# Kernel optimization log

Measured on AMD Instinct MI355X. Metric: run time of the kernel, lower is better.

The kernel has to match this reference:

```python
import jax, jax.numpy as jnp
import numpy as np

N_STATE = 1024
N_HEAD = 16
B = 2
S = 2048


def setup_inputs() -> dict:
    key = jax.random.key(0)
    ks = jax.random.split(key, 8)
    s = 0.02
    x = jax.random.normal(ks[0], (B, S, N_STATE), dtype=jnp.float32)
    # causal additive mask, as in Whisper: upper triangle = -inf
    mask = jnp.where(jnp.triu(jnp.ones((S, S), dtype=bool), k=1), -jnp.inf, 0.0).astype(jnp.float32)
    Wq = jax.random.normal(ks[1], (N_STATE, N_STATE), dtype=jnp.float32) * s
    bq = jax.random.normal(ks[2], (N_STATE,), dtype=jnp.float32) * s
    Wk = jax.random.normal(ks[3], (N_STATE, N_STATE), dtype=jnp.float32) * s
    Wv = jax.random.normal(ks[4], (N_STATE, N_STATE), dtype=jnp.float32) * s
    bv = jax.random.normal(ks[5], (N_STATE,), dtype=jnp.float32) * s
    Wo = jax.random.normal(ks[6], (N_STATE, N_STATE), dtype=jnp.float32) * s
    bo = jax.random.normal(ks[7], (N_STATE,), dtype=jnp.float32) * s
    return {"x": x, "mask": mask, "Wq": Wq, "bq": bq, "Wk": Wk,
            "Wv": Wv, "bv": bv, "Wo": Wo, "bo": bo}


def reference(x, mask, Wq, bq, Wk, Wv, bv, Wo, bo):
    Bb, S_, D = x.shape
    H = N_HEAD
    hd = D // H
    scale = hd ** (-0.25)  # scale split across q and k, as in the source
    q = x @ Wq.T + bq              # [B,S,D]
    k = x @ Wk.T                   # key has no bias
    v = x @ Wv.T + bv
    # [B,S,D] -> [B,H,S,hd]
    q = q.reshape(Bb, S_, H, hd).transpose(0, 2, 1, 3) * scale
    k = k.reshape(Bb, S_, H, hd).transpose(0, 2, 1, 3) * scale
    v = v.reshape(Bb, S_, H, hd).transpose(0, 2, 1, 3)
    qk = jnp.einsum('bhsd,bhtd->bhst', q, k) + mask[:S_, :S_]
    w = jax.nn.softmax(qk, axis=-1).astype(q.dtype)
    out = jnp.einsum('bhst,bhtd->bhsd', w, v)
    out = out.transpose(0, 2, 1, 3).reshape(Bb, S_, D)
    return out @ Wo.T + bo
```

## Files before the change

kernel.cpp:

```cpp
#include <hip/hip_runtime.h>
#include <hip/hip_bf16.h>
#include <cmath>

typedef __bf16 bf16;
typedef __bf16 bf16x8 __attribute__((ext_vector_type(8)));
typedef __bf16 bf16x4 __attribute__((ext_vector_type(4)));
typedef float f32x4 __attribute__((ext_vector_type(4)));

#define QS 0.18033688f

__device__ __forceinline__ void load16_to_lds(const void* g, void* l) {
    __builtin_amdgcn_global_load_lds(
        (const __attribute__((address_space(1))) unsigned int*)g,
        (__attribute__((address_space(3))) unsigned int*)l, 16, 0, 0);
}

__global__ __launch_bounds__(256) void convert_kernel(
    const float* __restrict__ x,  const float* __restrict__ wq,
    const float* __restrict__ wk, const float* __restrict__ wv,
    const float* __restrict__ wo, bf16* __restrict__ dst)
{
    const size_t M1 = 1024ull * 1024ull, M4 = 4ull * M1;
    size_t i0 = ((size_t)blockIdx.x * 256 + threadIdx.x) * 8;
    const float* s;
    size_t off;
    float sc = 1.f;
    if      (i0 < M4)        { s = x;  off = i0; }
    else if (i0 < M4 + M1)   { s = wq; off = i0 - M4; sc = QS; }
    else if (i0 < M4 + 2*M1) { s = wk; off = i0 - M4 - M1; }
    else if (i0 < M4 + 3*M1) { s = wv; off = i0 - M4 - 2*M1; }
    else                     { s = wo; off = i0 - M4 - 3*M1; }
    float4 a = *(const float4*)(s + off);
    float4 b = *(const float4*)(s + off + 4);
    bf16x8 r = { (bf16)(a.x*sc), (bf16)(a.y*sc), (bf16)(a.z*sc), (bf16)(a.w*sc),
                 (bf16)(b.x*sc), (bf16)(b.y*sc), (bf16)(b.z*sc), (bf16)(b.w*sc) };
    *(bf16x8*)(dst + i0) = r;
}

template<int BM, bool OUT_F32>
__device__ __forceinline__ void gemm_core(
    const bf16* __restrict__ A, const bf16* __restrict__ W,
    const float* __restrict__ bias, void* __restrict__ C,
    int mb, int nb, bool vt_out, float bias_scale)
{
    constexpr int IF = BM / 32;
    __shared__ __align__(16) bf16 As[BM * 32];
    __shared__ __align__(16) bf16 Bs[128 * 32];

    const int tid  = threadIdx.x;
    const int lane = tid & 63;
    const int wave = tid >> 6;
    const int wr   = (wave >> 1) * (BM / 2);
    const int wc   = (wave & 1) * 64;
    const int l15  = lane & 15;
    const int l4   = lane >> 4;
    const int swz  = (l4 ^ ((l15 >> 1) & 3)) * 8;

    f32x4 acc[IF][4] = {};

    for (int kt = 0; kt < 32; ++kt) {
#pragma unroll
        for (int it = 0; it < BM / 64; ++it) {
            int c = it * 256 + tid;
            int scol = ((c & 3) ^ ((c >> 3) & 3)) * 8;
            load16_to_lds(&A[(size_t)(mb * BM + (c >> 2)) * 1024 + kt * 32 + scol],
                          &As[(it * 256 + (tid & 192)) * 8]);
        }
#pragma unroll
        for (int it = 0; it < 2; ++it) {
            int c = it * 256 + tid;
            int scol = ((c & 3) ^ ((c >> 3) & 3)) * 8;
            load16_to_lds(&W[(size_t)(nb * 128 + (c >> 2)) * 1024 + kt * 32 + scol],
                          &Bs[(it * 256 + (tid & 192)) * 8]);
        }
        __syncthreads();
        bf16x8 af[IF], bfr[4];
#pragma unroll
        for (int i = 0; i < IF; ++i)
            af[i] = *(const bf16x8*)&As[(wr + i * 16 + l15) * 32 + swz];
#pragma unroll
        for (int j = 0; j < 4; ++j)
            bfr[j] = *(const bf16x8*)&Bs[(wc + j * 16 + l15) * 32 + swz];
#pragma unroll
        for (int i = 0; i < IF; ++i)
#pragma unroll
            for (int j = 0; j < 4; ++j)
                acc[i][j] = __builtin_amdgcn_mfma_f32_16x16x32_bf16(
                    af[i], bfr[j], acc[i][j], 0, 0, 0);
        __syncthreads();
    }

    if (!OUT_F32 && vt_out) {
#pragma unroll
        for (int j = 0; j < 4; ++j) {
            int col = nb * 128 + wc + j * 16 + l15;
            float bv = bias ? bias[col] : 0.f;
            int h = col >> 6, d = col & 63;
#pragma unroll
            for (int i = 0; i < IF; ++i) {
                int m0 = mb * BM + wr + i * 16 + l4 * 4;
                int b = m0 >> 11, s = m0 & 2047;
                bf16x4 pk = { (bf16)(acc[i][j][0] + bv), (bf16)(acc[i][j][1] + bv),
                              (bf16)(acc[i][j][2] + bv), (bf16)(acc[i][j][3] + bv) };
                *(bf16x4*)&((bf16*)C)[(size_t)((b * 16 + h) * 64 + d) * 2048 + s] = pk;
            }
        }
    } else {
#pragma unroll
        for (int j = 0; j < 4; ++j) {
            int col = nb * 128 + wc + j * 16 + l15;
            float bv = bias ? bias[col] * bias_scale : 0.f;
#pragma unroll
            for (int i = 0; i < IF; ++i) {
                int row0 = mb * BM + wr + i * 16 + l4 * 4;
#pragma unroll
                for (int r = 0; r < 4; ++r) {
                    float val = acc[i][j][r] + bv;
                    size_t idx = (size_t)(row0 + r) * 1024 + col;
                    if (OUT_F32) ((float*)C)[idx] = val;
                    else         ((bf16*)C)[idx]  = (bf16)val;
                }
            }
        }
    }
}

__global__ __launch_bounds__(256) void qkv_kernel(
    const bf16* __restrict__ xb,
    const bf16* __restrict__ wqb, const float* __restrict__ bq,
    const bf16* __restrict__ wkb,
    const bf16* __restrict__ wvb, const float* __restrict__ bv,
    bf16* __restrict__ q, bf16* __restrict__ k, bf16* __restrict__ vt)
{
    int mb = blockIdx.x;
    int nbg = blockIdx.y;
    int sel = nbg >> 3, nb = nbg & 7;
    const bf16* W = (sel == 0) ? wqb : ((sel == 1) ? wkb : wvb);
    const float* bias = (sel == 0) ? bq : ((sel == 2) ? bv : nullptr);
    bf16* C = (sel == 0) ? q : ((sel == 1) ? k : vt);
    gemm_core<128, false>(xb, W, bias, C, mb, nb, sel == 2,
                          sel == 0 ? QS : 1.f);
}

__global__ __launch_bounds__(256) void oproj_kernel(
    const bf16* __restrict__ ao, const bf16* __restrict__ wob,
    const float* __restrict__ bo, float* __restrict__ out)
{
    gemm_core<64, true>(ao, wob, bo, out, blockIdx.x, blockIdx.y, false, 1.f);
}

__global__ __launch_bounds__(256) void attn_kernel(
    const bf16* __restrict__ q, const bf16* __restrict__ k,
    const bf16* __restrict__ vt, bf16* __restrict__ o)
{
    __shared__ __align__(16) bf16 Ks[2][64 * 64];
    __shared__ __align__(16) bf16 Vs[2][64 * 64];
    __shared__ __align__(16) bf16 Ps[4][16 * 72];

    const int tid  = threadIdx.x;
    const int lane = tid & 63;
    const int wave = tid >> 6;
    const int l15  = lane & 15;
    const int l4   = lane >> 4;

    const int bh = blockIdx.x;
    const int pairIdx = blockIdx.y;
    const int b = bh >> 4, h = bh & 15;
    const int qts[2] = { pairIdx, 31 - pairIdx };

    auto stage = [&](int nt, int buf) {
#pragma unroll
        for (int it = 0; it < 2; ++it) {
            int c = it * 256 + tid;
            int scol = ((c & 7) ^ ((c >> 3) & 7)) * 8;
            load16_to_lds(&k[(size_t)(b * 2048 + nt * 64 + (c >> 3)) * 1024 + h * 64 + scol],
                          &Ks[buf][(it * 256 + (tid & 192)) * 8]);
            load16_to_lds(&vt[(size_t)(bh * 64 + (c >> 3)) * 2048 + nt * 64 + scol],
                          &Vs[buf][(it * 256 + (tid & 192)) * 8]);
        }
    };

    int b0 = 0;
    stage(0, 0);

    for (int seg = 0; seg < 2; ++seg) {
        const int qt = qts[seg];
        const int qg = qt * 64 + wave * 16 + l15;
        bf16x8 qf[2];
#pragma unroll
        for (int kk = 0; kk < 2; ++kk)
            qf[kk] = *(const bf16x8*)&q[(size_t)(b * 2048 + qg) * 1024 + h * 64 + kk * 32 + l4 * 8];

        f32x4 oacc[4] = {};
        float lsum = 0.f;

        const int n = qt + 1;
        for (int nt = 0; nt < n; ++nt) {
            __syncthreads();
            if (nt + 1 < n)      stage(nt + 1, b0 ^ 1);
            else if (seg == 0)   stage(0, b0 ^ 1);

            f32x4 s[4] = {};
#pragma unroll
            for (int kk = 0; kk < 2; ++kk) {
#pragma unroll
                for (int j = 0; j < 4; ++j) {
                    bf16x8 kf = *(const bf16x8*)&Ks[b0][(j * 16 + l15) * 64
                                    + (((kk * 4 + l4) ^ (l15 & 7)) * 8)];
                    s[j] = __builtin_amdgcn_mfma_f32_16x16x32_bf16(kf, qf[kk], s[j], 0, 0, 0);
                }
            }

            float pv[4][4];
            if (nt == qt) {
#pragma unroll
                for (int j = 0; j < 4; ++j)
#pragma unroll
                    for (int r = 0; r < 4; ++r) {
                        int kg = nt * 64 + j * 16 + l4 * 4 + r;
                        pv[j][r] = (kg > qg) ? 0.f : __builtin_amdgcn_exp2f(s[j][r]);
                    }
            } else {
#pragma unroll
                for (int j = 0; j < 4; ++j)
#pragma unroll
                    for (int r = 0; r < 4; ++r)
                        pv[j][r] = __builtin_amdgcn_exp2f(s[j][r]);
            }
#pragma unroll
            for (int j = 0; j < 4; ++j)
                lsum += (pv[j][0] + pv[j][1]) + (pv[j][2] + pv[j][3]);

#pragma unroll
            for (int j = 0; j < 4; ++j) {
                bf16x4 pk = { (bf16)pv[j][0], (bf16)pv[j][1], (bf16)pv[j][2], (bf16)pv[j][3] };
                *(bf16x4*)&Ps[wave][l15 * 72 + j * 16 + l4 * 4] = pk;
            }

#pragma unroll
            for (int kk = 0; kk < 2; ++kk) {
                bf16x8 pf = *(const bf16x8*)&Ps[wave][l15 * 72 + kk * 32 + l4 * 8];
#pragma unroll
                for (int f = 0; f < 4; ++f) {
                    bf16x8 vf = *(const bf16x8*)&Vs[b0][(f * 16 + l15) * 64
                                    + (((kk * 4 + l4) ^ (l15 & 7)) * 8)];
                    oacc[f] = __builtin_amdgcn_mfma_f32_16x16x32_bf16(pf, vf, oacc[f], 0, 0, 0);
                }
            }
            b0 ^= 1;
        }

        lsum += __shfl_xor(lsum, 16, 64);
        lsum += __shfl_xor(lsum, 32, 64);
        float rinv[4];
#pragma unroll
        for (int r = 0; r < 4; ++r) rinv[r] = 1.f / __shfl(lsum, l4 * 4 + r, 64);
#pragma unroll
        for (int f = 0; f < 4; ++f)
#pragma unroll
            for (int r = 0; r < 4; ++r)
                o[(size_t)(b * 2048 + qt * 64 + wave * 16 + l4 * 4 + r) * 1024 + h * 64 + f * 16 + l15]
                    = (bf16)(oacc[f][r] * rinv[r]);
    }
}

extern "C" void kernel_launch(void* const* d_in, const int* in_sizes, int n_in,
                              void* d_out, int out_size, void* d_ws, size_t ws_size,
                              hipStream_t stream)
{
    const float* x  = (const float*)d_in[0];
    const float* Wq = (const float*)d_in[2];
    const float* bq = (const float*)d_in[3];
    const float* Wk = (const float*)d_in[4];
    const float* Wv = (const float*)d_in[5];
    const float* bv = (const float*)d_in[6];
    const float* Wo = (const float*)d_in[7];
    const float* bo = (const float*)d_in[8];
    float* out = (float*)d_out;

    const size_t M1 = 1024ull * 1024ull, M4 = 4ull * M1;
    bf16* base = (bf16*)d_ws;
    bf16* xb  = base;
    bf16* wqb = base + M4;
    bf16* wkb = base + M4 + M1;
    bf16* wvb = base + M4 + 2 * M1;
    bf16* wob = base + M4 + 3 * M1;
    bf16* q   = base + 8 * M1;
    bf16* k   = base + 12 * M1;
    bf16* vt  = base + 16 * M1;
    bf16* ao  = xb;

    convert_kernel<<<4096, 256, 0, stream>>>(x, Wq, Wk, Wv, Wo, base);
    qkv_kernel<<<dim3(32, 24), 256, 0, stream>>>(xb, wqb, bq, wkb, wvb, bv, q, k, vt);
    attn_kernel<<<dim3(32, 16), 256, 0, stream>>>(q, k, vt, ao);
    oproj_kernel<<<dim3(64, 8), 256, 0, stream>>>(ao, wob, bo, out);
}
```

Measured before the change: 184.5 us.

## Process 128-row query tiles per attention block to share K/V tiles

Each attention block now handles two adjacent 64-row query sub-tiles together instead of two mirrored tiles one after the other. Every K/V tile staged in LDS is used by both sub-tiles, which roughly halves K/V loads and barriers per query row, and the diagonal sub-tile's MFMAs are skipped where it is fully masked. The cost is more register pressure (two sets of Q fragments, accumulators and scores) and a weaker causal load balance: work per block now ranges from 2 to 32 tiles, where the old mirrored pairing gave every block the same amount. A launch-bounds occupancy hint of 3 blocks per CU is also added.

```diff
diff --git a/kernel.cpp b/kernel.cpp
--- a/kernel.cpp
+++ b/kernel.cpp
@@ -149,13 +149,13 @@
     gemm_core<64, true>(ao, wob, bo, out, blockIdx.x, blockIdx.y, false, 1.f);
 }
 
-__global__ __launch_bounds__(256) void attn_kernel(
+__global__ __launch_bounds__(256, 3) void attn_kernel(
     const bf16* __restrict__ q, const bf16* __restrict__ k,
     const bf16* __restrict__ vt, bf16* __restrict__ o)
 {
     __shared__ __align__(16) bf16 Ks[2][64 * 64];
     __shared__ __align__(16) bf16 Vs[2][64 * 64];
-    __shared__ __align__(16) bf16 Ps[4][16 * 72];
+    __shared__ __align__(16) bf16 Ps[4][2][16 * 72];
 
     const int tid  = threadIdx.x;
     const int lane = tid & 63;
@@ -164,9 +164,11 @@
     const int l4   = lane >> 4;
 
     const int bh = blockIdx.x;
-    const int pairIdx = blockIdx.y;
+    const int y  = blockIdx.y;
+    const int qt2 = (y < 8) ? y : (23 - y);
     const int b = bh >> 4, h = bh & 15;
-    const int qts[2] = { pairIdx, 31 - pairIdx };
+    const int q0 = qt2 * 128;
+    const int nTiles = 2 * qt2 + 2;
 
     auto stage = [&](int nt, int buf) {
 #pragma unroll
@@ -180,87 +182,101 @@
         }
     };
 
+    bf16x8 qf[2][2];
+    int qg[2];
+#pragma unroll
+    for (int f = 0; f < 2; ++f) {
+        qg[f] = q0 + f * 64 + wave * 16 + l15;
+#pragma unroll
+        for (int kk = 0; kk < 2; ++kk)
+            qf[f][kk] = *(const bf16x8*)&q[(size_t)(b * 2048 + qg[f]) * 1024 + h * 64 + kk * 32 + l4 * 8];
+    }
+
+    f32x4 oacc[2][4] = {};
+    float lsum[2] = {0.f, 0.f};
     int b0 = 0;
     stage(0, 0);
 
-    for (int seg = 0; seg < 2; ++seg) {
-        const int qt = qts[seg];
-        const int qg = qt * 64 + wave * 16 + l15;
-        bf16x8 qf[2];
-#pragma unroll
-        for (int kk = 0; kk < 2; ++kk)
-            qf[kk] = *(const bf16x8*)&q[(size_t)(b * 2048 + qg) * 1024 + h * 64 + kk * 32 + l4 * 8];
-
-        f32x4 oacc[4] = {};
-        float lsum = 0.f;
-
-        const int n = qt + 1;
-        for (int nt = 0; nt < n; ++nt) {
-            __syncthreads();
-            if (nt + 1 < n)      stage(nt + 1, b0 ^ 1);
-            else if (seg == 0)   stage(0, b0 ^ 1);
-
-            f32x4 s[4] = {};
-#pragma unroll
-            for (int kk = 0; kk < 2; ++kk) {
-#pragma unroll
-                for (int j = 0; j < 4; ++j) {
-                    bf16x8 kf = *(const bf16x8*)&Ks[b0][(j * 16 + l15) * 64
-                                    + (((kk * 4 + l4) ^ (l15 & 7)) * 8)];
-                    s[j] = __builtin_amdgcn_mfma_f32_16x16x32_bf16(kf, qf[kk], s[j], 0, 0, 0);
-                }
-            }
-
+    for (int nt = 0; nt < nTiles; ++nt) {
+        __syncthreads();
+        if (nt + 1 < nTiles) stage(nt + 1, b0 ^ 1);
+
+        const bool a0 = (nt <= 2 * qt2);
+
+        f32x4 s[2][4] = {};
+#pragma unroll
+        for (int kk = 0; kk < 2; ++kk) {
+#pragma unroll
+            for (int j = 0; j < 4; ++j) {
+                bf16x8 kf = *(const bf16x8*)&Ks[b0][(j * 16 + l15) * 64
+                                + (((kk * 4 + l4) ^ (l15 & 7)) * 8)];
+                s[1][j] = __builtin_amdgcn_mfma_f32_16x16x32_bf16(kf, qf[1][kk], s[1][j], 0, 0, 0);
+                if (a0)
+                    s[0][j] = __builtin_amdgcn_mfma_f32_16x16x32_bf16(kf, qf[0][kk], s[0][j], 0, 0, 0);
+            }
+        }
+
+#pragma unroll
+        for (int f = 0; f < 2; ++f) {
+            if (f == 0 && !a0) continue;
             float pv[4][4];
-            if (nt == qt) {
+            if (nt == 2 * qt2 + f) {
 #pragma unroll
                 for (int j = 0; j < 4; ++j)
 #pragma unroll
                     for (int r = 0; r < 4; ++r) {
                         int kg = nt * 64 + j * 16 + l4 * 4 + r;
-                        pv[j][r] = (kg > qg) ? 0.f : __builtin_amdgcn_exp2f(s[j][r]);
+                        pv[j][r] = (kg > qg[f]) ? 0.f : __builtin_amdgcn_exp2f(s[f][j][r]);
                     }
             } else {
 #pragma unroll
                 for (int j = 0; j < 4; ++j)
 #pragma unroll
                     for (int r = 0; r < 4; ++r)
-                        pv[j][r] = __builtin_amdgcn_exp2f(s[j][r]);
+                        pv[j][r] = __builtin_amdgcn_exp2f(s[f][j][r]);
             }
 #pragma unroll
             for (int j = 0; j < 4; ++j)
-                lsum += (pv[j][0] + pv[j][1]) + (pv[j][2] + pv[j][3]);
+                lsum[f] += (pv[j][0] + pv[j][1]) + (pv[j][2] + pv[j][3]);
 
 #pragma unroll
             for (int j = 0; j < 4; ++j) {
                 bf16x4 pk = { (bf16)pv[j][0], (bf16)pv[j][1], (bf16)pv[j][2], (bf16)pv[j][3] };
-                *(bf16x4*)&Ps[wave][l15 * 72 + j * 16 + l4 * 4] = pk;
-            }
-
-#pragma unroll
-            for (int kk = 0; kk < 2; ++kk) {
-                bf16x8 pf = *(const bf16x8*)&Ps[wave][l15 * 72 + kk * 32 + l4 * 8];
-#pragma unroll
-                for (int f = 0; f < 4; ++f) {
-                    bf16x8 vf = *(const bf16x8*)&Vs[b0][(f * 16 + l15) * 64
-                                    + (((kk * 4 + l4) ^ (l15 & 7)) * 8)];
-                    oacc[f] = __builtin_amdgcn_mfma_f32_16x16x32_bf16(pf, vf, oacc[f], 0, 0, 0);
-                }
-            }
-            b0 ^= 1;
-        }
-
-        lsum += __shfl_xor(lsum, 16, 64);
-        lsum += __shfl_xor(lsum, 32, 64);
+                *(bf16x4*)&Ps[wave][f][l15 * 72 + j * 16 + l4 * 4] = pk;
+            }
+        }
+
+#pragma unroll
+        for (int kk = 0; kk < 2; ++kk) {
+            bf16x8 pf1 = *(const bf16x8*)&Ps[wave][1][l15 * 72 + kk * 32 + l4 * 8];
+            bf16x8 pf0 = *(const bf16x8*)&Ps[wave][0][l15 * 72 + kk * 32 + l4 * 8];
+#pragma unroll
+            for (int fi = 0; fi < 4; ++fi) {
+                bf16x8 vf = *(const bf16x8*)&Vs[b0][(fi * 16 + l15) * 64
+                                + (((kk * 4 + l4) ^ (l15 & 7)) * 8)];
+                oacc[1][fi] = __builtin_amdgcn_mfma_f32_16x16x32_bf16(pf1, vf, oacc[1][fi], 0, 0, 0);
+                if (a0)
+                    oacc[0][fi] = __builtin_amdgcn_mfma_f32_16x16x32_bf16(pf0, vf, oacc[0][fi], 0, 0, 0);
+            }
+        }
+        b0 ^= 1;
+    }
+
+#pragma unroll
+    for (int f = 0; f < 2; ++f) {
+        float ls = lsum[f];
+        ls += __shfl_xor(ls, 16, 64);
+        ls += __shfl_xor(ls, 32, 64);
         float rinv[4];
 #pragma unroll
-        for (int r = 0; r < 4; ++r) rinv[r] = 1.f / __shfl(lsum, l4 * 4 + r, 64);
-#pragma unroll
-        for (int f = 0; f < 4; ++f)
+        for (int r = 0; r < 4; ++r) rinv[r] = 1.f / __shfl(ls, l4 * 4 + r, 64);
+#pragma unroll
+        for (int fi = 0; fi < 4; ++fi)
 #pragma unroll
             for (int r = 0; r < 4; ++r)
-                o[(size_t)(b * 2048 + qt * 64 + wave * 16 + l4 * 4 + r) * 1024 + h * 64 + f * 16 + l15]
-                    = (bf16)(oacc[f][r] * rinv[r]);
+                o[(size_t)(b * 2048 + q0 + f * 64 + wave * 16 + l4 * 4 + r) * 1024
+                  + h * 64 + fi * 16 + l15]
+                    = (bf16)(oacc[f][fi][r] * rinv[r]);
     }
 }
 
```

Result: slower. 197.8 us (+7.2%).
